# Kernel tuning notes

Measured on AMD Instinct MI355X. Metric: run time of the kernel, lower is better.

Reference implementation:

```python
import jax, jax.numpy as jnp
import numpy as np

B, S, D, V, K, H, L, U = 256, 50, 32, 10000, 16, 64, 2, 32
NORM = 0.01


def setup_inputs() -> dict:
    key = jax.random.key(0)
    ks = iter(jax.random.split(key, 64))
    r = lambda *sh: jax.random.normal(next(ks), sh, dtype=jnp.float32) * 0.05
    inp = {
        'x1': r(B, U), 'z1': r(B, S, D), 'x2': r(B, U), 'z2': r(B, S, D),
        'embd': r(V, D),
        'dec_w1': r(D, H), 'dec_b1': r(H), 'dec_w2': r(H, D), 'dec_b2': r(D),
        'i_wih': r(3 * D, D), 'i_whh': r(3 * D, D), 'i_bih': r(3 * D), 'i_bhh': r(3 * D),
        'c_wih': r(3 * D, D), 'c_whh': r(3 * D, D), 'c_bih': r(3 * D), 'c_bhh': r(3 * D),
        'im_w1': r(D, D), 'im_b1': r(D), 'im_w2': r(D, D), 'im_b2': r(D),
        'cm_w1': r(D, D), 'cm_b1': r(D), 'cm_w2': r(D, D), 'cm_b2': r(D),
        'hw1': r(L, D, K * K), 'hb1': r(L, K * K), 'hw2': r(L, D, K * K), 'hb2': r(L, K * K),
        'lin_w': r(L, U, K), 'lin_b': r(L, K), 'lout_w': r(L, K, U), 'lout_b': r(L, U),
        'sample_num': B, 'trigger_seq_length': 30,
    }
    return inp


def _gru(x, wih, whh, bih, bhh):
    # PyTorch GRU, batch_first, h0 = 0; gate order (r, z, n)
    gi = jnp.einsum('bsd,ed->bse', x, wih) + bih  # [B,S,3D]

    def step(h, gi_t):
        gh = h @ whh.T + bhh
        gir, giz, gin = jnp.split(gi_t, 3, axis=-1)
        ghr, ghz, ghn = jnp.split(gh, 3, axis=-1)
        rr = jax.nn.sigmoid(gir + ghr)
        zz = jax.nn.sigmoid(giz + ghz)
        nn = jnp.tanh(gin + rr * ghn)
        h = (1.0 - zz) * nn + zz * h
        return h, h

    h0 = jnp.zeros((x.shape[0], whh.shape[1]), x.dtype)
    _, hs = jax.lax.scan(step, h0, jnp.swapaxes(gi, 0, 1))
    return jnp.swapaxes(hs, 0, 1)  # [B,S,D]


def _forward(x1, z1, x2, z2, embd, dec_w1, dec_b1, dec_w2, dec_b2,
             i_wih, i_whh, i_bih, i_bhh, c_wih, c_whh, c_bih, c_bhh,
             im_w1, im_b1, im_w2, im_b2, cm_w1, cm_b1, cm_w2, cm_b2,
             hw1, hb1, hw2, hb2, lin_w, lin_b, lout_w, lout_b,
             sample_num, trigger_seq_length):
    # --- VQVAE.find_nearest: cdist + argmin + gather (index path has no grad) ---
    q = jax.lax.stop_gradient(z1)
    t = jax.lax.stop_gradient(embd)
    # ||q - t||^2 expanded; argmin over sqrt == argmin over squared dist
    d2 = ((q * q).sum(-1)[:, :, None]
          - 2.0 * jnp.einsum('bsd,vd->bsv', q, t)
          + (t * t).sum(-1)[None, None, :])  # [B,S,V]
    idx = jnp.argmin(d2, axis=2)  # [B,S]
    z_emb = embd[idx]  # [B,S,D], gradient flows into embd via gather

    # --- VQVAE.decode ---
    h = jax.nn.leaky_relu(z_emb @ dec_w1 + dec_b1, negative_slope=0.1)
    z_recon = h @ dec_w2 + dec_b2  # [B,S,D]

    total_loss = jnp.mean((z2 - jax.lax.stop_gradient(z_emb)) ** 2)

    # --- item branch: GRU -> pick trigger step -> MLP (tanh, linear) ---
    hs = _gru(z_recon, i_wih, i_whh, i_bih, i_bhh)
    u1 = hs[:, trigger_seq_length, :]
    z1f = jnp.tanh(u1 @ im_w1 + im_b1) @ im_w2 + im_b2  # [B,D]

    # --- category branch ---
    hs = _gru(z2, c_wih, c_whh, c_bih, c_bhh)
    u2 = hs[:, trigger_seq_length, :]
    z2f = jnp.tanh(u2 @ cm_w1 + cm_b1) @ cm_w2 + cm_b2  # [B,D]

    # --- hypernetwork layers (activations in self.modules are never applied) ---
    out = x1
    for i in range(L):
        iw = (z1f @ hw1[i] + hb1[i]).reshape(sample_num, K, K)
        cw = (z2f @ hw2[i] + hb2[i]).reshape(sample_num, K, K)
        w = jnp.clip(iw, -NORM, NORM) + cw  # [B,K,K]
        out = out @ lin_w[i] + lin_b[i]  # [B,K]
        out = jnp.einsum('bk,bkj->bj', out, w)  # bmm
        out = out @ lout_w[i] + lout_b[i]  # [B,U]
    return out, total_loss


def reference(x1, z1, x2, z2, embd, dec_w1, dec_b1, dec_w2, dec_b2,
              i_wih, i_whh, i_bih, i_bhh, c_wih, c_whh, c_bih, c_bhh,
              im_w1, im_b1, im_w2, im_b2, cm_w1, cm_b1, cm_w2, cm_b2,
              hw1, hb1, hw2, hb2, lin_w, lin_b, lout_w, lout_b,
              sample_num, trigger_seq_length):
    return _forward(x1, z1, x2, z2, embd, dec_w1, dec_b1, dec_w2, dec_b2,
                    i_wih, i_whh, i_bih, i_bhh, c_wih, c_whh, c_bih, c_bhh,
                    im_w1, im_b1, im_w2, im_b2, cm_w1, cm_b1, cm_w2, cm_b2,
                    hw1, hb1, hw2, hb2, lin_w, lin_b, lout_w, lout_b,
                    sample_num, trigger_seq_length)
```

## Files before the change

kernel.cpp:

```cpp
#include <hip/hip_runtime.h>
#include <math.h>

#define B 256
#define S 50
#define D 32
#define V 10000
#define VPAD 10240
#define KK 16
#define HH 64
#define LL 2
#define UU 32
#define TT 30
#define NROWS (B*S)
#define NORMC 0.01f
#define CH 256
#define NSLICE 8
#define SLICE_V 1280
#define VQ_RB 128

typedef __attribute__((ext_vector_type(8))) short bf16x8;
typedef __attribute__((ext_vector_type(4))) float f32x4;

__device__ __forceinline__ float sigmoidf_(float x) { return 1.0f / (1.0f + expf(-x)); }

__device__ __forceinline__ unsigned short f2bf(float x) {
    union { float f; unsigned int u; } a; a.f = x;
    unsigned int u = a.u;
    return (unsigned short)((u + 0x7FFFu + ((u >> 16) & 1u)) >> 16);
}
__device__ __forceinline__ float bf2f(unsigned short h) {
    union { unsigned int u; float f; } a; a.u = ((unsigned int)h) << 16; return a.f;
}

__device__ __forceinline__ void gld16(void* lds, const void* g) {
    __builtin_amdgcn_global_load_lds(
        (const __attribute__((address_space(1))) unsigned int*)g,
        (__attribute__((address_space(3))) unsigned int*)lds, 16, 0, 0);
}
__device__ __forceinline__ void gld4(void* lds, const void* g) {
    __builtin_amdgcn_global_load_lds(
        (const __attribute__((address_space(1))) unsigned int*)g,
        (__attribute__((address_space(3))) unsigned int*)lds, 4, 0, 0);
}

__global__ __launch_bounds__(256) void k_prep(const float* __restrict__ embd,
                                              const float* __restrict__ z1,
                                              unsigned short* __restrict__ Eh, unsigned short* __restrict__ El,
                                              unsigned short* __restrict__ Qh, unsigned short* __restrict__ Ql,
                                              float* __restrict__ tn, float* __restrict__ loss_sum) {
    int gid = blockIdx.x * 256 + threadIdx.x;
    if (gid == 0) loss_sum[0] = 0.f;
    if (gid >= VPAD * 4 + 4 * NROWS) return;
    int isRow = (gid >= VPAD * 4);
    if (!isRow) {
        int item = gid >> 2, qd = gid & 3;
        unsigned short* dh = Eh + (size_t)item * D + qd * 8;
        unsigned short* dl = El + (size_t)item * D + qd * 8;
        if (item >= V) {
            unsigned short z[8] = {0, 0, 0, 0, 0, 0, 0, 0};
            *(uint4*)dh = *(const uint4*)z;
            *(uint4*)dl = *(const uint4*)z;
            if (qd == 0) tn[item] = INFINITY;
            return;
        }
        const float* src = embd + (size_t)item * D + qd * 8;
        float4 x0 = *(const float4*)(src);
        float4 x1 = *(const float4*)(src + 4);
        float xs[8] = {x0.x, x0.y, x0.z, x0.w, x1.x, x1.y, x1.z, x1.w};
        unsigned short hv[8], lv[8];
        float ss = 0.f;
#pragma unroll
        for (int i = 0; i < 8; i++) {
            float x = xs[i];
            ss = fmaf(x, x, ss);
            unsigned short h = f2bf(x);
            hv[i] = h;
            lv[i] = f2bf(x - bf2f(h));
        }
        *(uint4*)dh = *(const uint4*)hv;
        *(uint4*)dl = *(const uint4*)lv;
        ss += __shfl_xor(ss, 1);
        ss += __shfl_xor(ss, 2);
        if (qd == 0) tn[item] = 0.5f * ss;
    } else {
        int g = gid - VPAD * 4;
        int item = g >> 2, qd = g & 3;
        const float* src = z1 + (size_t)item * D + qd * 8;
        unsigned short* dh = Qh + (size_t)item * D + qd * 8;
        unsigned short* dl = Ql + (size_t)item * D + qd * 8;
        float4 x0 = *(const float4*)(src);
        float4 x1 = *(const float4*)(src + 4);
        float xs[8] = {x0.x, x0.y, x0.z, x0.w, x1.x, x1.y, x1.z, x1.w};
        unsigned short hv[8], lv[8];
#pragma unroll
        for (int i = 0; i < 8; i++) {
            float x = -xs[i];
            unsigned short h = f2bf(x);
            hv[i] = h;
            lv[i] = f2bf(x - bf2f(h));
        }
        *(uint4*)dh = *(const uint4*)hv;
        *(uint4*)dl = *(const uint4*)lv;
    }
}

__global__ __launch_bounds__(256) void k_vq(const short* __restrict__ Qh, const short* __restrict__ Ql,
                                            const short* __restrict__ Eh, const short* __restrict__ El,
                                            const float* __restrict__ tn,
                                            float* __restrict__ pb_s, int* __restrict__ pb_v) {
    __shared__ __attribute__((aligned(16))) short EhL[CH * 32];
    __shared__ __attribute__((aligned(16))) short ElL[CH * 32];
    __shared__ float tnL[CH];
    const int tid = threadIdx.x;
    const int wave = tid >> 6, lane = tid & 63;
    const int rg = blockIdx.x >> 3, slice = blockIdx.x & 7;
    const int row0 = rg * VQ_RB;
    const int quad = lane >> 4, c15 = lane & 15;
    const int swz = quad ^ ((c15 >> 1) & 3);
    const int ar0 = row0 + wave * 32 + c15;
    bf16x8 ah0 = *(const bf16x8*)(Qh + (size_t)ar0 * 32 + quad * 8);
    bf16x8 al0 = *(const bf16x8*)(Ql + (size_t)ar0 * 32 + quad * 8);
    bf16x8 ah1 = *(const bf16x8*)(Qh + (size_t)(ar0 + 16) * 32 + quad * 8);
    bf16x8 al1 = *(const bf16x8*)(Ql + (size_t)(ar0 + 16) * 32 + quad * 8);
    float best0[4], best1[4]; int bv0[4], bv1[4];
#pragma unroll
    for (int i = 0; i < 4; i++) {
        best0[i] = INFINITY; best1[i] = INFINITY;
        bv0[i] = 0x7fffffff; bv1[i] = 0x7fffffff;
    }
    const int vbeg = slice * SLICE_V;
    for (int c0 = 0; c0 < SLICE_V; c0 += CH) {
        __syncthreads();
        {
            const int sbS = (vbeg + c0) * 32;
#pragma unroll
            for (int i = 0; i < 4; i++) {
                int c = wave * 256 + i * 64 + lane;
                int code = c >> 2;
                int q = (c & 3) ^ ((c >> 3) & 3);
                int srcOff = sbS + code * 32 + q * 8;
                int dstOff = (wave * 256 + i * 64) * 8;
                gld16(EhL + dstOff, Eh + srcOff);
                gld16(ElL + dstOff, El + srcOff);
            }
            gld4(tnL + wave * 64, tn + vbeg + c0 + wave * 64 + lane);
        }
        __syncthreads();
#pragma unroll
        for (int t = 0; t < 16; t++) {
            const int code = t * 16 + c15;
            const int boff = code * 32 + swz * 8;
            bf16x8 bh = *(const bf16x8*)(EhL + boff);
            bf16x8 bl = *(const bf16x8*)(ElL + boff);
            const float tnv = tnL[code];
            f32x4 acc0 = {tnv, tnv, tnv, tnv};
            f32x4 acc1 = {tnv, tnv, tnv, tnv};
            acc0 = __builtin_amdgcn_mfma_f32_16x16x32_bf16(ah0, bh, acc0, 0, 0, 0);
            acc1 = __builtin_amdgcn_mfma_f32_16x16x32_bf16(ah1, bh, acc1, 0, 0, 0);
            acc0 = __builtin_amdgcn_mfma_f32_16x16x32_bf16(al0, bh, acc0, 0, 0, 0);
            acc1 = __builtin_amdgcn_mfma_f32_16x16x32_bf16(al1, bh, acc1, 0, 0, 0);
            acc0 = __builtin_amdgcn_mfma_f32_16x16x32_bf16(ah0, bl, acc0, 0, 0, 0);
            acc1 = __builtin_amdgcn_mfma_f32_16x16x32_bf16(ah1, bl, acc1, 0, 0, 0);
            acc0 = __builtin_amdgcn_mfma_f32_16x16x32_bf16(al0, bl, acc0, 0, 0, 0);
            acc1 = __builtin_amdgcn_mfma_f32_16x16x32_bf16(al1, bl, acc1, 0, 0, 0);
            const int v = vbeg + c0 + code;
#pragma unroll
            for (int i = 0; i < 4; i++) {
                float s0 = acc0[i];
                if (s0 < best0[i]) { best0[i] = s0; bv0[i] = v; }
                float s1 = acc1[i];
                if (s1 < best1[i]) { best1[i] = s1; bv1[i] = v; }
            }
        }
    }
#pragma unroll
    for (int m = 1; m <= 8; m <<= 1) {
#pragma unroll
        for (int i = 0; i < 4; i++) {
            float os = __shfl_xor(best0[i], m); int ov = __shfl_xor(bv0[i], m);
            if (os < best0[i] || (os == best0[i] && ov < bv0[i])) { best0[i] = os; bv0[i] = ov; }
            os = __shfl_xor(best1[i], m); ov = __shfl_xor(bv1[i], m);
            if (os < best1[i] || (os == best1[i] && ov < bv1[i])) { best1[i] = os; bv1[i] = ov; }
        }
    }
    if (c15 == 0) {
#pragma unroll
        for (int i = 0; i < 4; i++) {
            int r0 = row0 + wave * 32 + quad * 4 + i;
            pb_s[(size_t)r0 * NSLICE + slice] = best0[i];
            pb_v[(size_t)r0 * NSLICE + slice] = bv0[i];
            int r1 = r0 + 16;
            pb_s[(size_t)r1 * NSLICE + slice] = best1[i];
            pb_v[(size_t)r1 * NSLICE + slice] = bv1[i];
        }
    }
}

__global__ __launch_bounds__(256) void k_gather(const float* __restrict__ z2,
                                                const float* __restrict__ embd,
                                                const float* __restrict__ pb_s,
                                                const int* __restrict__ pb_v,
                                                const float* __restrict__ dw1,
                                                const float* __restrict__ db1,
                                                const float* __restrict__ dw2,
                                                const float* __restrict__ db2,
                                                float* __restrict__ z_recon,
                                                float* __restrict__ loss_sum) {
    __shared__ float dw1L[2048];
    __shared__ float dw2L[2048];
    __shared__ float db1L[64], db2L[32];
    __shared__ int   vidL[32];
    __shared__ float zeL[32][33];
    __shared__ float aL[32][65];
    const int tid = threadIdx.x;
    const int row0 = blockIdx.x * 32;
    for (int p = tid; p < 2048; p += 256) { dw1L[p] = dw1[p]; dw2L[p] = dw2[p]; }
    if (tid < 64) db1L[tid] = db1[tid];
    if (tid >= 64 && tid < 96) db2L[tid - 64] = db2[tid - 64];
    if (tid < 32) {
        const int r = row0 + tid;
        float bs = INFINITY; int bv = 0x7fffffff;
#pragma unroll
        for (int j = 0; j < NSLICE; j++) {
            float s = pb_s[(size_t)r * NSLICE + j];
            int   v = pb_v[(size_t)r * NSLICE + j];
            if (s < bs) { bs = s; bv = v; }
        }
        vidL[tid] = bv;
    }
    __syncthreads();
    const int r = tid >> 3, q = tid & 7;
    {
        float4 e4 = *(const float4*)(embd + (size_t)vidL[r] * D + q * 4);
        zeL[r][q * 4 + 0] = e4.x; zeL[r][q * 4 + 1] = e4.y;
        zeL[r][q * 4 + 2] = e4.z; zeL[r][q * 4 + 3] = e4.w;
    }
    __syncthreads();
    {
        const float* zp = z2 + (size_t)(row0 + r) * D + q * 4;
        float4 x4 = *(const float4*)zp;
        float d0 = x4.x - zeL[r][q * 4 + 0], d1 = x4.y - zeL[r][q * 4 + 1];
        float d2 = x4.z - zeL[r][q * 4 + 2], d3 = x4.w - zeL[r][q * 4 + 3];
        float ls = d0 * d0 + d1 * d1 + d2 * d2 + d3 * d3;
#pragma unroll
        for (int off = 32; off > 0; off >>= 1) ls += __shfl_down(ls, off);
        if ((tid & 63) == 0) atomicAdd(loss_sum, ls);
    }
    const int s = (row0 + r) % S;
    const bool dec = (s <= TT);
    if (dec) {
#pragma unroll
        for (int j = 0; j < 8; j++) {
            int h = q * 8 + j;
            float a = db1L[h];
#pragma unroll
            for (int d = 0; d < 32; d++) a = fmaf(zeL[r][d], dw1L[d * 64 + h], a);
            aL[r][h] = (a >= 0.f) ? a : 0.1f * a;
        }
    }
    __syncthreads();
    if (dec) {
        const int b = (row0 + r) / S;
        float zr[4];
#pragma unroll
        for (int dd = 0; dd < 4; dd++) zr[dd] = db2L[q * 4 + dd];
        for (int h = 0; h < 64; h++) {
            float av = aL[r][h];
#pragma unroll
            for (int dd = 0; dd < 4; dd++) zr[dd] = fmaf(av, dw2L[h * 32 + q * 4 + dd], zr[dd]);
        }
        float4 o4 = make_float4(zr[0], zr[1], zr[2], zr[3]);
        *(float4*)(z_recon + (size_t)b * ((TT + 1) * D) + s * D + q * 4) = o4;
    }
}

__global__ __launch_bounds__(128) void k_gru(const float* __restrict__ z_recon,
                                             const float* __restrict__ z2,
                                             const float* __restrict__ i_wih, const float* __restrict__ i_whh,
                                             const float* __restrict__ i_bih, const float* __restrict__ i_bhh,
                                             const float* __restrict__ c_wih, const float* __restrict__ c_whh,
                                             const float* __restrict__ c_bih, const float* __restrict__ c_bhh,
                                             const float* __restrict__ im_w1, const float* __restrict__ im_b1,
                                             const float* __restrict__ im_w2, const float* __restrict__ im_b2,
                                             const float* __restrict__ cm_w1, const float* __restrict__ cm_b1,
                                             const float* __restrict__ cm_w2, const float* __restrict__ cm_b2,
                                             float* __restrict__ z1f, float* __restrict__ z2f) {
    const int tid = threadIdx.x;
    const int which = blockIdx.x >> 8;
    const int b = blockIdx.x & 255;
    const float* x; int xstride;
    const float *wih, *whh, *bih, *bhh, *w1, *b1, *w2, *b2; float* zf;
    if (which == 0) { x = z_recon; xstride = (TT + 1) * D; wih = i_wih; whh = i_whh; bih = i_bih; bhh = i_bhh; w1 = im_w1; b1 = im_b1; w2 = im_w2; b2 = im_b2; zf = z1f; }
    else            { x = z2;      xstride = S * D;        wih = c_wih; whh = c_whh; bih = c_bih; bhh = c_bhh; w1 = cm_w1; b1 = cm_b1; w2 = cm_w2; b2 = cm_b2; zf = z2f; }
    __shared__ float wihT[32][97];
    __shared__ float whhT[32][97];
    __shared__ float gi[TT + 1][96];
    __shared__ float xs[TT + 1][32];
    __shared__ float hsh[2][32];
    __shared__ float gh[96];
    __shared__ float bh2[96];
    __shared__ float af[32];
    for (int p = tid; p < 96 * 32; p += 128) {
        int e = p >> 5, d = p & 31;
        wihT[d][e] = wih[p];
        whhT[d][e] = whh[p];
    }
    for (int p = tid; p < (TT + 1) * D; p += 128) xs[p >> 5][p & 31] = x[(size_t)b * xstride + p];
    if (tid < 96) bh2[tid] = bhh[tid];
    if (tid < 32) hsh[0][tid] = 0.f;
    __syncthreads();
    for (int p = tid; p < (TT + 1) * 96; p += 128) {
        int s = p / 96, e = p % 96;
        float g0 = bih[e], g1 = 0.f;
#pragma unroll
        for (int d = 0; d < 16; d++) g0 = fmaf(xs[s][d], wihT[d][e], g0);
#pragma unroll
        for (int d = 16; d < 32; d++) g1 = fmaf(xs[s][d], wihT[d][e], g1);
        gi[s][e] = g0 + g1;
    }
    __syncthreads();
    for (int t = 0; t <= TT; t++) {
        const int cur = t & 1;
        if (tid < 96) {
            float g0 = bh2[tid], g1 = 0.f;
#pragma unroll
            for (int d = 0; d < 16; d++) g0 = fmaf(hsh[cur][d], whhT[d][tid], g0);
#pragma unroll
            for (int d = 16; d < 32; d++) g1 = fmaf(hsh[cur][d], whhT[d][tid], g1);
            gh[tid] = g0 + g1;
        }
        __syncthreads();
        if (tid < 32) {
            float rr = sigmoidf_(gi[t][tid] + gh[tid]);
            float zz = sigmoidf_(gi[t][tid + 32] + gh[tid + 32]);
            float nn = tanhf(gi[t][tid + 64] + rr * gh[tid + 64]);
            hsh[1 - cur][tid] = (1.f - zz) * nn + zz * hsh[cur][tid];
        }
        __syncthreads();
    }
    if (tid < 32) {
        float a = b1[tid];
#pragma unroll
        for (int d = 0; d < 32; d++) a = fmaf(hsh[1][d], w1[d * 32 + tid], a);
        af[tid] = tanhf(a);
    }
    __syncthreads();
    if (tid < 32) {
        float o = b2[tid];
#pragma unroll
        for (int d = 0; d < 32; d++) o = fmaf(af[d], w2[d * 32 + tid], o);
        zf[(size_t)b * 32 + tid] = o;
    }
}

__global__ __launch_bounds__(256) void k_wgen(const float* __restrict__ z1f_, const float* __restrict__ z2f_,
                                              const float* __restrict__ hw1, const float* __restrict__ hb1,
                                              const float* __restrict__ hw2, const float* __restrict__ hb2,
                                              float* __restrict__ w_out) {
    __shared__ float z1s[32], z2s[32];
    const int tid = threadIdx.x;
    const int b = blockIdx.x >> 1;
    const int layer = blockIdx.x & 1;
    if (tid < 32) z1s[tid] = z1f_[b * 32 + tid];
    else if (tid < 64) z2s[tid - 32] = z2f_[b * 32 + tid - 32];
    __syncthreads();
    const int kk = tid;
    const float* h1 = hw1 + layer * 8192 + kk;
    const float* h2 = hw2 + layer * 8192 + kk;
    float a = hb1[layer * 256 + kk];
    float c = hb2[layer * 256 + kk];
#pragma unroll
    for (int d = 0; d < 32; d++) {
        a = fmaf(z1s[d], h1[d * 256], a);
        c = fmaf(z2s[d], h2[d * 256], c);
    }
    a = fminf(fmaxf(a, -NORMC), NORMC);
    w_out[(size_t)b * 512 + layer * 256 + kk] = a + c;
}

__global__ __launch_bounds__(256) void k_apply(const float* __restrict__ x1,
                                               const float* __restrict__ w_in,
                                               const float* __restrict__ lin_w, const float* __restrict__ lin_b,
                                               const float* __restrict__ lout_w, const float* __restrict__ lout_b,
                                               const float* __restrict__ loss_sum, float* __restrict__ out) {
    __shared__ float linw[1024], loutw[1024], linb[32], loutb[64];
    __shared__ float wL[8][512];
    __shared__ float oc[8][32], t1s[8][16], t2s[8][16];
    const int tid = threadIdx.x;
    const int b0 = blockIdx.x * 8;
    {
        for (int p = tid; p < 1024; p += 256) { linw[p] = lin_w[p]; loutw[p] = lout_w[p]; }
        if (tid < 32) linb[tid] = lin_b[tid];
        if (tid >= 32 && tid < 96) loutb[tid - 32] = lout_b[tid - 32];
        const float4* src = (const float4*)(w_in + (size_t)b0 * 512);
#pragma unroll
        for (int i = 0; i < 4; i++) {
            float4 v = src[tid + i * 256];
            ((float4*)&wL[0][0])[tid + i * 256] = v;
        }
        float v = x1[b0 * 32 + tid];
        oc[tid >> 5][tid & 31] = v;
    }
    __syncthreads();
    const int s = tid >> 5, l = tid & 31;
#pragma unroll
    for (int i = 0; i < LL; i++) {
        if (l < 16) {
            float a = linb[i * 16 + l];
#pragma unroll
            for (int u = 0; u < 32; u++) a = fmaf(oc[s][u], linw[i * 512 + u * 16 + l], a);
            t1s[s][l] = a;
        }
        __syncthreads();
        if (l < 16) {
            float a = 0.f;
#pragma unroll
            for (int k = 0; k < 16; k++) a = fmaf(t1s[s][k], wL[s][i * 256 + k * 16 + l], a);
            t2s[s][l] = a;
        }
        __syncthreads();
        {
            float a = loutb[i * 32 + l];
#pragma unroll
            for (int k = 0; k < 16; k++) a = fmaf(t2s[s][k], loutw[i * 512 + k * 32 + l], a);
            oc[s][l] = a;
        }
        __syncthreads();
    }
    out[(size_t)(b0 + s) * 32 + l] = oc[s][l];
    if (blockIdx.x == 0 && tid == 0) out[B * UU] = loss_sum[0] * (1.0f / (float)(B * S * D));
}

extern "C" void kernel_launch(void* const* d_in, const int* in_sizes, int n_in,
                              void* d_out, int out_size, void* d_ws, size_t ws_size,
                              hipStream_t stream) {
    const float* x1     = (const float*)d_in[0];
    const float* z1     = (const float*)d_in[1];
    const float* z2     = (const float*)d_in[3];
    const float* embd   = (const float*)d_in[4];
    const float* dec_w1 = (const float*)d_in[5];
    const float* dec_b1 = (const float*)d_in[6];
    const float* dec_w2 = (const float*)d_in[7];
    const float* dec_b2 = (const float*)d_in[8];
    const float* i_wih  = (const float*)d_in[9];
    const float* i_whh  = (const float*)d_in[10];
    const float* i_bih  = (const float*)d_in[11];
    const float* i_bhh  = (const float*)d_in[12];
    const float* c_wih  = (const float*)d_in[13];
    const float* c_whh  = (const float*)d_in[14];
    const float* c_bih  = (const float*)d_in[15];
    const float* c_bhh  = (const float*)d_in[16];
    const float* im_w1  = (const float*)d_in[17];
    const float* im_b1  = (const float*)d_in[18];
    const float* im_w2  = (const float*)d_in[19];
    const float* im_b2  = (const float*)d_in[20];
    const float* cm_w1  = (const float*)d_in[21];
    const float* cm_b1  = (const float*)d_in[22];
    const float* cm_w2  = (const float*)d_in[23];
    const float* cm_b2  = (const float*)d_in[24];
    const float* hw1    = (const float*)d_in[25];
    const float* hb1    = (const float*)d_in[26];
    const float* hw2    = (const float*)d_in[27];
    const float* hb2    = (const float*)d_in[28];
    const float* lin_w  = (const float*)d_in[29];
    const float* lin_b  = (const float*)d_in[30];
    const float* lout_w = (const float*)d_in[31];
    const float* lout_b = (const float*)d_in[32];

    float* wsf      = (float*)d_ws;
    float* loss_sum = wsf;
    float* tn       = wsf + 64;
    float* pb_s     = wsf + 10304;
    int*   pb_v     = (int*)(wsf + 112704);
    unsigned short* Eh = (unsigned short*)(wsf + 215104);
    unsigned short* El = (unsigned short*)(wsf + 378944);
    unsigned short* Qh = (unsigned short*)(wsf + 542784);
    unsigned short* Ql = (unsigned short*)(wsf + 747584);
    float* z1f      = wsf + 952384;
    float* z2f      = wsf + 960576;
    float* z_recon  = (float*)Eh;
    float* w_out    = (float*)Qh;

    k_prep<<<(VPAD * 4 + 4 * NROWS + 255) / 256, 256, 0, stream>>>(embd, z1, Eh, El, Qh, Ql, tn, loss_sum);
    k_vq<<<(NROWS / VQ_RB) * NSLICE, 256, 0, stream>>>((const short*)Qh, (const short*)Ql,
                                                       (const short*)Eh, (const short*)El, tn, pb_s, pb_v);
    k_gather<<<NROWS / 32, 256, 0, stream>>>(z2, embd, pb_s, pb_v, dec_w1, dec_b1,
                                             dec_w2, dec_b2, z_recon, loss_sum);
    k_gru<<<512, 128, 0, stream>>>(z_recon, z2, i_wih, i_whh, i_bih, i_bhh,
                                   c_wih, c_whh, c_bih, c_bhh,
                                   im_w1, im_b1, im_w2, im_b2,
                                   cm_w1, cm_b1, cm_w2, cm_b2, z1f, z2f);
    k_wgen<<<2 * B, 256, 0, stream>>>(z1f, z2f, hw1, hb1, hw2, hb2, w_out);
    k_apply<<<B / 8, 256, 0, stream>>>(x1, w_out, lin_w, lin_b, lout_w, lout_b,
                                       loss_sum, (float*)d_out);
}
```

Baseline: 245.6 us.

## Keep codebook tiles in registers and stream query rows in VQ argmin

The VQ nearest-code kernel is restructured so each wave holds 256 codebook entries (hi/lo bf16 plus norms) in registers and streams 256 query rows past them. This removes the LDS staging and block barriers. The low×low MFMA term is dropped, leaving three MFMAs per tile instead of four, which slightly lowers split-bf16 precision. Partial results now cover 40 code groups and are stored as packed float2 pairs, and the gather kernel reduces them in parallel across 8 lanes with shuffles. The cost is higher register pressure and a larger partial-result buffer.

After: 257.3 us. 4.8% more time.

```diff
diff --git a/kernel.cpp b/kernel.cpp
--- a/kernel.cpp
+++ b/kernel.cpp
@@ -13,10 +13,11 @@
 #define TT 30
 #define NROWS (B*S)
 #define NORMC 0.01f
-#define CH 256
-#define NSLICE 8
-#define SLICE_V 1280
-#define VQ_RB 128
+#define NCG 40
+#define CPW 256
+#define NTILE 16
+#define ROWCH 50
+#define RPC 256
 
 typedef __attribute__((ext_vector_type(8))) short bf16x8;
 typedef __attribute__((ext_vector_type(4))) float f32x4;
@@ -30,17 +31,6 @@
 }
 __device__ __forceinline__ float bf2f(unsigned short h) {
     union { unsigned int u; float f; } a; a.u = ((unsigned int)h) << 16; return a.f;
-}
-
-__device__ __forceinline__ void gld16(void* lds, const void* g) {
-    __builtin_amdgcn_global_load_lds(
-        (const __attribute__((address_space(1))) unsigned int*)g,
-        (__attribute__((address_space(3))) unsigned int*)lds, 16, 0, 0);
-}
-__device__ __forceinline__ void gld4(void* lds, const void* g) {
-    __builtin_amdgcn_global_load_lds(
-        (const __attribute__((address_space(1))) unsigned int*)g,
-        (__attribute__((address_space(3))) unsigned int*)lds, 4, 0, 0);
 }
 
 __global__ __launch_bounds__(256) void k_prep(const float* __restrict__ embd,
@@ -107,99 +97,66 @@
 __global__ __launch_bounds__(256) void k_vq(const short* __restrict__ Qh, const short* __restrict__ Ql,
                                             const short* __restrict__ Eh, const short* __restrict__ El,
                                             const float* __restrict__ tn,
-                                            float* __restrict__ pb_s, int* __restrict__ pb_v) {
-    __shared__ __attribute__((aligned(16))) short EhL[CH * 32];
-    __shared__ __attribute__((aligned(16))) short ElL[CH * 32];
-    __shared__ float tnL[CH];
+                                            float2* __restrict__ pbsv) {
     const int tid = threadIdx.x;
-    const int wave = tid >> 6, lane = tid & 63;
-    const int rg = blockIdx.x >> 3, slice = blockIdx.x & 7;
-    const int row0 = rg * VQ_RB;
+    const int lane = tid & 63;
+    const int gw = blockIdx.x * 4 + (tid >> 6);
+    const int cg = gw % NCG, rc = gw / NCG;
     const int quad = lane >> 4, c15 = lane & 15;
-    const int swz = quad ^ ((c15 >> 1) & 3);
-    const int ar0 = row0 + wave * 32 + c15;
-    bf16x8 ah0 = *(const bf16x8*)(Qh + (size_t)ar0 * 32 + quad * 8);
-    bf16x8 al0 = *(const bf16x8*)(Ql + (size_t)ar0 * 32 + quad * 8);
-    bf16x8 ah1 = *(const bf16x8*)(Qh + (size_t)(ar0 + 16) * 32 + quad * 8);
-    bf16x8 al1 = *(const bf16x8*)(Ql + (size_t)(ar0 + 16) * 32 + quad * 8);
-    float best0[4], best1[4]; int bv0[4], bv1[4];
-#pragma unroll
-    for (int i = 0; i < 4; i++) {
-        best0[i] = INFINITY; best1[i] = INFINITY;
-        bv0[i] = 0x7fffffff; bv1[i] = 0x7fffffff;
-    }
-    const int vbeg = slice * SLICE_V;
-    for (int c0 = 0; c0 < SLICE_V; c0 += CH) {
-        __syncthreads();
-        {
-            const int sbS = (vbeg + c0) * 32;
-#pragma unroll
-            for (int i = 0; i < 4; i++) {
-                int c = wave * 256 + i * 64 + lane;
-                int code = c >> 2;
-                int q = (c & 3) ^ ((c >> 3) & 3);
-                int srcOff = sbS + code * 32 + q * 8;
-                int dstOff = (wave * 256 + i * 64) * 8;
-                gld16(EhL + dstOff, Eh + srcOff);
-                gld16(ElL + dstOff, El + srcOff);
+    const int code0 = cg * CPW;
+    bf16x8 bh[NTILE], bl[NTILE];
+    float tnr[NTILE];
+#pragma unroll
+    for (int i = 0; i < NTILE; i++) {
+        const int code = code0 + i * 16 + c15;
+        bh[i] = *(const bf16x8*)(Eh + (size_t)code * 32 + quad * 8);
+        bl[i] = *(const bf16x8*)(El + (size_t)code * 32 + quad * 8);
+        tnr[i] = tn[code];
+    }
+    for (int step = 0; step < RPC / 16; step++) {
+        const int row0 = rc * RPC + step * 16;
+        const bf16x8 ah = *(const bf16x8*)(Qh + (size_t)(row0 + c15) * 32 + quad * 8);
+        const bf16x8 al = *(const bf16x8*)(Ql + (size_t)(row0 + c15) * 32 + quad * 8);
+        float best[4]; int bestv[4];
+#pragma unroll
+        for (int e = 0; e < 4; e++) { best[e] = INFINITY; bestv[e] = 0x7fffffff; }
+#pragma unroll
+        for (int i = 0; i < NTILE; i++) {
+            const float t0 = tnr[i];
+            f32x4 acc = {t0, t0, t0, t0};
+            acc = __builtin_amdgcn_mfma_f32_16x16x32_bf16(ah, bh[i], acc, 0, 0, 0);
+            acc = __builtin_amdgcn_mfma_f32_16x16x32_bf16(al, bh[i], acc, 0, 0, 0);
+            acc = __builtin_amdgcn_mfma_f32_16x16x32_bf16(ah, bl[i], acc, 0, 0, 0);
+            const int v = code0 + i * 16 + c15;
+#pragma unroll
+            for (int e = 0; e < 4; e++) {
+                float s = acc[e];
+                if (s < best[e]) { best[e] = s; bestv[e] = v; }
             }
-            gld4(tnL + wave * 64, tn + vbeg + c0 + wave * 64 + lane);
-        }
-        __syncthreads();
-#pragma unroll
-        for (int t = 0; t < 16; t++) {
-            const int code = t * 16 + c15;
-            const int boff = code * 32 + swz * 8;
-            bf16x8 bh = *(const bf16x8*)(EhL + boff);
-            bf16x8 bl = *(const bf16x8*)(ElL + boff);
-            const float tnv = tnL[code];
-            f32x4 acc0 = {tnv, tnv, tnv, tnv};
-            f32x4 acc1 = {tnv, tnv, tnv, tnv};
-            acc0 = __builtin_amdgcn_mfma_f32_16x16x32_bf16(ah0, bh, acc0, 0, 0, 0);
-            acc1 = __builtin_amdgcn_mfma_f32_16x16x32_bf16(ah1, bh, acc1, 0, 0, 0);
-            acc0 = __builtin_amdgcn_mfma_f32_16x16x32_bf16(al0, bh, acc0, 0, 0, 0);
-            acc1 = __builtin_amdgcn_mfma_f32_16x16x32_bf16(al1, bh, acc1, 0, 0, 0);
-            acc0 = __builtin_amdgcn_mfma_f32_16x16x32_bf16(ah0, bl, acc0, 0, 0, 0);
-            acc1 = __builtin_amdgcn_mfma_f32_16x16x32_bf16(ah1, bl, acc1, 0, 0, 0);
-            acc0 = __builtin_amdgcn_mfma_f32_16x16x32_bf16(al0, bl, acc0, 0, 0, 0);
-            acc1 = __builtin_amdgcn_mfma_f32_16x16x32_bf16(al1, bl, acc1, 0, 0, 0);
-            const int v = vbeg + c0 + code;
-#pragma unroll
-            for (int i = 0; i < 4; i++) {
-                float s0 = acc0[i];
-                if (s0 < best0[i]) { best0[i] = s0; bv0[i] = v; }
-                float s1 = acc1[i];
-                if (s1 < best1[i]) { best1[i] = s1; bv1[i] = v; }
+        }
+#pragma unroll
+        for (int m = 1; m <= 8; m <<= 1) {
+#pragma unroll
+            for (int e = 0; e < 4; e++) {
+                float os = __shfl_xor(best[e], m);
+                int   ov = __shfl_xor(bestv[e], m);
+                if (os < best[e] || (os == best[e] && ov < bestv[e])) { best[e] = os; bestv[e] = ov; }
             }
         }
-    }
-#pragma unroll
-    for (int m = 1; m <= 8; m <<= 1) {
-#pragma unroll
-        for (int i = 0; i < 4; i++) {
-            float os = __shfl_xor(best0[i], m); int ov = __shfl_xor(bv0[i], m);
-            if (os < best0[i] || (os == best0[i] && ov < bv0[i])) { best0[i] = os; bv0[i] = ov; }
-            os = __shfl_xor(best1[i], m); ov = __shfl_xor(bv1[i], m);
-            if (os < best1[i] || (os == best1[i] && ov < bv1[i])) { best1[i] = os; bv1[i] = ov; }
-        }
-    }
-    if (c15 == 0) {
-#pragma unroll
-        for (int i = 0; i < 4; i++) {
-            int r0 = row0 + wave * 32 + quad * 4 + i;
-            pb_s[(size_t)r0 * NSLICE + slice] = best0[i];
-            pb_v[(size_t)r0 * NSLICE + slice] = bv0[i];
-            int r1 = r0 + 16;
-            pb_s[(size_t)r1 * NSLICE + slice] = best1[i];
-            pb_v[(size_t)r1 * NSLICE + slice] = bv1[i];
+        if (c15 == 0) {
+#pragma unroll
+            for (int e = 0; e < 4; e++) {
+                const int row = row0 + quad * 4 + e;
+                float2 p; p.x = best[e]; p.y = __int_as_float(bestv[e]);
+                pbsv[(size_t)row * NCG + cg] = p;
+            }
         }
     }
 }
 
 __global__ __launch_bounds__(256) void k_gather(const float* __restrict__ z2,
                                                 const float* __restrict__ embd,
-                                                const float* __restrict__ pb_s,
-                                                const int* __restrict__ pb_v,
+                                                const float2* __restrict__ pbsv,
                                                 const float* __restrict__ dw1,
                                                 const float* __restrict__ db1,
                                                 const float* __restrict__ dw2,
@@ -217,19 +174,24 @@
     for (int p = tid; p < 2048; p += 256) { dw1L[p] = dw1[p]; dw2L[p] = dw2[p]; }
     if (tid < 64) db1L[tid] = db1[tid];
     if (tid >= 64 && tid < 96) db2L[tid - 64] = db2[tid - 64];
-    if (tid < 32) {
-        const int r = row0 + tid;
+    const int r = tid >> 3, q = tid & 7;
+    {
         float bs = INFINITY; int bv = 0x7fffffff;
 #pragma unroll
-        for (int j = 0; j < NSLICE; j++) {
-            float s = pb_s[(size_t)r * NSLICE + j];
-            int   v = pb_v[(size_t)r * NSLICE + j];
-            if (s < bs) { bs = s; bv = v; }
-        }
-        vidL[tid] = bv;
-    }
-    __syncthreads();
-    const int r = tid >> 3, q = tid & 7;
+        for (int j = 0; j < NCG / 8; j++) {
+            float2 p = pbsv[(size_t)(row0 + r) * NCG + j * 8 + q];
+            int v = __float_as_int(p.y);
+            if (p.x < bs || (p.x == bs && v < bv)) { bs = p.x; bv = v; }
+        }
+#pragma unroll
+        for (int m = 1; m <= 4; m <<= 1) {
+            float os = __shfl_xor(bs, m);
+            int   ov = __shfl_xor(bv, m);
+            if (os < bs || (os == bs && ov < bv)) { bs = os; bv = ov; }
+        }
+        if (q == 0) vidL[r] = bv;
+    }
+    __syncthreads();
     {
         float4 e4 = *(const float4*)(embd + (size_t)vidL[r] * D + q * 4);
         zeL[r][q * 4 + 0] = e4.x; zeL[r][q * 4 + 1] = e4.y;
@@ -470,21 +432,20 @@
     float* wsf      = (float*)d_ws;
     float* loss_sum = wsf;
     float* tn       = wsf + 64;
-    float* pb_s     = wsf + 10304;
-    int*   pb_v     = (int*)(wsf + 112704);
-    unsigned short* Eh = (unsigned short*)(wsf + 215104);
-    unsigned short* El = (unsigned short*)(wsf + 378944);
-    unsigned short* Qh = (unsigned short*)(wsf + 542784);
-    unsigned short* Ql = (unsigned short*)(wsf + 747584);
-    float* z1f      = wsf + 952384;
-    float* z2f      = wsf + 960576;
+    float2* pbsv    = (float2*)(wsf + 10304);
+    unsigned short* Eh = (unsigned short*)(wsf + 1034304);
+    unsigned short* El = (unsigned short*)(wsf + 1198144);
+    unsigned short* Qh = (unsigned short*)(wsf + 1361984);
+    unsigned short* Ql = (unsigned short*)(wsf + 1566784);
+    float* z1f      = wsf + 1771584;
+    float* z2f      = wsf + 1779776;
     float* z_recon  = (float*)Eh;
     float* w_out    = (float*)Qh;
 
     k_prep<<<(VPAD * 4 + 4 * NROWS + 255) / 256, 256, 0, stream>>>(embd, z1, Eh, El, Qh, Ql, tn, loss_sum);
-    k_vq<<<(NROWS / VQ_RB) * NSLICE, 256, 0, stream>>>((const short*)Qh, (const short*)Ql,
-                                                       (const short*)Eh, (const short*)El, tn, pb_s, pb_v);
-    k_gather<<<NROWS / 32, 256, 0, stream>>>(z2, embd, pb_s, pb_v, dec_w1, dec_b1,
+    k_vq<<<(NCG * ROWCH) / 4, 256, 0, stream>>>((const short*)Qh, (const short*)Ql,
+                                                (const short*)Eh, (const short*)El, tn, pbsv);
+    k_gather<<<NROWS / 32, 256, 0, stream>>>(z2, embd, pbsv, dec_w1, dec_b1,
                                              dec_w2, dec_b2, z_recon, loss_sum);
     k_gru<<<512, 128, 0, stream>>>(z_recon, z2, i_wih, i_whh, i_bih, i_bhh,
                                    c_wih, c_whh, c_bih, c_bhh,
```
